# Performance work log

Measured on AMD Instinct MI355X. Metric: run time of the kernel, lower is better.

The kernel has to match this reference:

```python
import jax, jax.numpy as jnp
import numpy as np

N, D, K = 65536, 128, 2048
ENTROPY_TEMP = 0.01


def setup_inputs() -> dict:
    key = jax.random.key(0)
    k1, k2 = jax.random.split(key, 2)
    x = jax.random.normal(k1, (N, D), dtype=jnp.float32)
    mask = jnp.ones((N,), dtype=jnp.float32)
    # variance_scaling(1.0, fan_in, uniform): U(-sqrt(3/fan_in), sqrt(3/fan_in))
    lim = np.sqrt(3.0 / D).astype(np.float32)
    codebook = jax.random.uniform(k2, (K, D), dtype=jnp.float32, minval=-lim, maxval=lim)
    return {"x": x, "mask": mask, "codebook": codebook}


def _entropy_loss(affinity, mask, temperature):
    # affinity: (N, K), mask: (N,)
    aff = affinity * mask[:, None] + (1.0 - mask[:, None]) * (-100000.0)
    aff = aff / temperature
    probs = jax.nn.softmax(aff, axis=-1)
    log_probs = jax.nn.log_softmax(aff + 1e-5, axis=-1)
    target_probs = probs  # loss_type == 'softmax'
    msum = jnp.sum(mask)
    avg_probs = jnp.sum(target_probs * mask[:, None], axis=0) / msum
    avg_entropy = -jnp.sum(avg_probs * jnp.log(avg_probs + 1e-5))
    sample_entropy = -jnp.sum(jnp.sum(target_probs * log_probs, axis=-1) * mask) / msum
    return sample_entropy - avg_entropy


def reference(x, mask, codebook):
    # --- l2_norm branch: normalize x rows ---
    xn = x + (1.0 - mask)[:, None] * 1e-6
    xn = xn / jnp.maximum(jnp.linalg.norm(xn, axis=-1, keepdims=True), 1e-6)
    # squared euclidean distance with a2 = b2 = 1.0 (per the l2_norm branch)
    distances = 2.0 - 2.0 * jnp.matmul(xn, codebook.T)  # (N, K)
    logits = -distances
    encoding_indices = jnp.argmax(logits, axis=-1)  # (N,)
    # quantize: one_hot @ codebook == gather
    quantized = jnp.take(codebook, encoding_indices, axis=0)  # (N, D)
    denom = jnp.sum(mask) + 1e-6
    # per-token squared distance between unit-norm vectors: 2 - 2 * <a, b>
    e_latent_loss = jnp.sum((2.0 - 2.0 * jnp.sum(jax.lax.stop_gradient(quantized) * xn, axis=-1)) * mask) / denom
    q_latent_loss = jnp.sum((2.0 - 2.0 * jnp.sum(quantized * jax.lax.stop_gradient(xn), axis=-1)) * mask) / denom
    entropy_loss = _entropy_loss(-distances, mask, ENTROPY_TEMP)
    # straight-through estimator
    quantized_st = xn + jax.lax.stop_gradient(quantized - xn)
    # bincount with float weights == segment_sum of mask
    code_count = jax.ops.segment_sum(mask, encoding_indices, num_segments=K).astype(jnp.float32)
    return (quantized_st,
            jnp.asarray(e_latent_loss, jnp.float32),
            jnp.asarray(q_latent_loss, jnp.float32),
            jnp.asarray(entropy_loss, jnp.float32),
            code_count,
            encoding_indices)
```

## Files before the change

kernel.cpp:

```cpp
#include <hip/hip_runtime.h>
#include <math.h>

#define NTOK 65536
#define DIMD 128
#define KCB  2048
#define NSLAB 512

typedef unsigned short u16;
typedef __attribute__((ext_vector_type(8))) unsigned short u16x8;
typedef __attribute__((ext_vector_type(8))) __bf16 bf16x8;
typedef __attribute__((ext_vector_type(4))) float f32x4;

union U8 { u16x8 u; bf16x8 b; };

__device__ __forceinline__ u16 f2bf(float f) {
  union { float f; unsigned u; } c; c.f = f;
  unsigned r = c.u + 0x7FFFu + ((c.u >> 16) & 1u);
  return (u16)(r >> 16);
}
__device__ __forceinline__ float keyval(int k) {
  union { int i; float f; } c; c.i = k & 0xFFFFF800;
  return c.f;
}
__device__ __forceinline__ int imax(int a, int b) { return a > b ? a : b; }
__device__ __forceinline__ int imin(int a, int b) { return a < b ? a : b; }

__device__ __forceinline__ void stage4(const char* srcLane, char* ldsWaveBase) {
  #pragma unroll
  for (int i = 0; i < 4; ++i)
    __builtin_amdgcn_global_load_lds((const __attribute__((address_space(1))) void*)(srcLane + i * 4096),
                                     (__attribute__((address_space(3))) void*)(ldsWaveBase + i * 4096), 16, 0, 0);
}


__global__ __launch_bounds__(256) void k_packcb(const float* __restrict__ cb, u16* __restrict__ cbp,
                                                float* __restrict__ acc4) {
  const int gid = blockIdx.x * 256 + threadIdx.x;
  if (gid == 0) { acc4[0] = 0.0f; acc4[1] = 0.0f; acc4[2] = 0.0f; acc4[3] = 0.0f; }
  if (gid >= 32768) return;
  const int lane = gid & 63;
  const int f = (gid >> 6) & 15;
  const int T = gid >> 10;
  const int ks = f >> 2, nf = f & 3;
  const int hi = lane >> 4, l15 = lane & 15;
  const int c = T * 64 + nf * 16 + l15;
  const int d0 = ks * 32 + hi * 8;
  const float4 v0 = *(const float4*)(cb + (size_t)c * DIMD + d0);
  const float4 v1 = *(const float4*)(cb + (size_t)c * DIMD + d0 + 4);
  const float e[8] = {v0.x, v0.y, v0.z, v0.w, v1.x, v1.y, v1.z, v1.w};
  union { u16 s[8]; u16x8 u; } oh;
  #pragma unroll
  for (int i = 0; i < 8; ++i) oh.s[i] = f2bf(e[i]);
  u16* tile = cbp + (size_t)T * 8192;
  *(u16x8*)(tile + (f * 64 + lane) * 8) = oh.u;
}


__global__ __launch_bounds__(256, 4) void k_pass1(const float* __restrict__ x, const float* __restrict__ mask,
                                                  const float* __restrict__ cb, const u16* __restrict__ cbp,
                                                  float* __restrict__ outQ, float* __restrict__ outEnc,
                                                  float* __restrict__ apPart, float* __restrict__ cnPart,
                                                  float* __restrict__ acc4) {
  __shared__ __align__(16) char Bsmem[32768];
  const int tid = threadIdx.x;
  const int lane = tid & 63, w = tid >> 6;
  const int l15 = lane & 15, hi = lane >> 4;
  const int row0 = blockIdx.x * 128;
  const char* src = (const char*)cbp;

  U8 Ah[2][4];
  #pragma unroll
  for (int mf = 0; mf < 2; ++mf) {
    const int row = row0 + w * 32 + mf * 16 + l15;
    const float add = (1.0f - mask[row]) * 1e-6f;
    const float* xr = x + (size_t)row * DIMD + hi * 8;
    float xf[4][8];
    float ss = 0.f;
    #pragma unroll
    for (int ks = 0; ks < 4; ++ks) {
      const float4 a = *(const float4*)(xr + ks * 32);
      const float4 bq = *(const float4*)(xr + ks * 32 + 4);
      xf[ks][0] = a.x + add;  xf[ks][1] = a.y + add;  xf[ks][2] = a.z + add;  xf[ks][3] = a.w + add;
      xf[ks][4] = bq.x + add; xf[ks][5] = bq.y + add; xf[ks][6] = bq.z + add; xf[ks][7] = bq.w + add;
      #pragma unroll
      for (int e = 0; e < 8; ++e) ss = fmaf(xf[ks][e], xf[ks][e], ss);
    }
    ss += __shfl_xor(ss, 16, 64);
    ss += __shfl_xor(ss, 32, 64);
    const float sc = 1.0f / fmaxf(sqrtf(ss), 1e-6f);
    #pragma unroll
    for (int ks = 0; ks < 4; ++ks) {
      union { u16 s[8]; u16x8 u; } th;
      #pragma unroll
      for (int e = 0; e < 8; ++e) th.s[e] = f2bf(xf[ks][e] * sc);
      Ah[mf][ks].u = th.u;
    }
  }

  int kv1[8], kv2[8];
  #pragma unroll
  for (int r = 0; r < 8; ++r) { kv1[r] = 0x80000000; kv2[r] = 0x80000000; }

  stage4(src + 0 * 16384 + tid * 16, Bsmem + 0 * 16384 + w * 1024);

  for (int t = 0; t < 32; ++t) {
    const int b = t & 1;
    asm volatile("s_waitcnt vmcnt(0)" ::: "memory");
    __builtin_amdgcn_sched_barrier(0);
    __builtin_amdgcn_s_barrier();
    __builtin_amdgcn_sched_barrier(0);
    if (t < 31)
      stage4(src + (size_t)(t + 1) * 16384 + tid * 16, Bsmem + (b ^ 1) * 16384 + w * 1024);

    const char* base = Bsmem + b * 16384 + lane * 16;
    f32x4 acc[2][4];
    #pragma unroll
    for (int m = 0; m < 2; ++m)
      #pragma unroll
      for (int nf = 0; nf < 4; ++nf) acc[m][nf] = (f32x4){0.f, 0.f, 0.f, 0.f};

    __builtin_amdgcn_s_setprio(1);
    #pragma unroll
    for (int ks = 0; ks < 4; ++ks) {
      #pragma unroll
      for (int nf = 0; nf < 4; ++nf) {
        U8 bh;
        bh.u = *(const u16x8*)(base + ((ks * 4 + nf) << 10));
        acc[0][nf] = __builtin_amdgcn_mfma_f32_16x16x32_bf16(Ah[0][ks].b, bh.b, acc[0][nf], 0, 0, 0);
        acc[1][nf] = __builtin_amdgcn_mfma_f32_16x16x32_bf16(Ah[1][ks].b, bh.b, acc[1][nf], 0, 0, 0);
      }
    }
    __builtin_amdgcn_s_setprio(0);

    const int base11 = t * 64 + l15;
    #pragma unroll
    for (int m = 0; m < 2; ++m)
      #pragma unroll
      for (int rg = 0; rg < 4; ++rg) {
        const int r = m * 4 + rg;
        int kk[4];
        #pragma unroll
        for (int nf = 0; nf < 4; ++nf) {
          union { float f; int i; } cv;
          cv.f = acc[m][nf][rg];
          kk[nf] = (cv.i & 0xFFFFF800) | (base11 + nf * 16);
        }
        const int h1 = imax(kk[0], kk[1]), lo1 = imin(kk[0], kk[1]);
        const int h2 = imax(kk[2], kk[3]), lo2 = imin(kk[2], kk[3]);
        const int t1 = imax(h1, h2);
        const int t2 = imax(imin(h1, h2), (h1 > h2) ? lo1 : lo2);
        kv2[r] = imax(imax(kv2[r], t2), imin(kv1[r], t1));
        kv1[r] = imax(kv1[r], t1);
      }
  }

  __syncthreads();
  float* apLds = (float*)Bsmem;
  float* cnLds = (float*)Bsmem + KCB;
  float* smr = (float*)Bsmem + 2 * KCB;
  for (int i = tid; i < 2 * KCB; i += 256) ((float*)Bsmem)[i] = 0.0f;
  __syncthreads();

  float msum = 0.f, slat = 0.f, sent = 0.f;
  #pragma unroll
  for (int m = 0; m < 2; ++m)
    #pragma unroll
    for (int rg = 0; rg < 4; ++rg) {
      const int r = m * 4 + rg;
      int a1k = kv1[r];
      #pragma unroll
      for (int off = 1; off <= 8; off <<= 1) {
        const int ok = __shfl_xor(a1k, off, 64);
        a1k = ok > a1k ? ok : a1k;
      }
      const float a1val = keyval(a1k);
      const float val1 = keyval(kv1[r]);
      const float val2 = keyval(kv2[r]);
      const int row = row0 + w * 32 + m * 16 + hi * 4 + rg;
      const float mk = mask[row];
      const float add = (1.0f - mk) * 1e-6f;
      const float* xr = x + (size_t)row * DIMD + l15 * 8;
      const float4 xa = *(const float4*)xr;
      const float4 xb = *(const float4*)(xr + 4);
      float xs0[8] = {xa.x + add, xa.y + add, xa.z + add, xa.w + add,
                      xb.x + add, xb.y + add, xb.z + add, xb.w + add};
      float ss = 0.f;
      #pragma unroll
      for (int e = 0; e < 8; ++e) ss = fmaf(xs0[e], xs0[e], ss);
      #pragma unroll
      for (int off = 1; off <= 8; off <<= 1) ss += __shfl_xor(ss, off, 64);
      const float sc = 1.0f / fmaxf(sqrtf(ss), 1e-6f);
      const float RT = 4e-3f;
      const bool f1 = val1 > a1val - RT;
      const bool f2 = val2 > a1val - RT;
      const unsigned long long b1 = __ballot(f1);
      const unsigned long long b2 = __ballot(f2);
      unsigned m1 = (unsigned)((b1 >> (hi * 16)) & 0xFFFFull);
      unsigned m2 = (unsigned)((b2 >> (hi * 16)) & 0xFFFFull);
      float bestd = -1e30f;
      int bestk = 0x7fffffff;
      while (m1) {
        const int s = __builtin_ctz(m1); m1 &= m1 - 1;
        const int kc = __shfl(kv1[r], (hi << 4) | s, 64) & 2047;
        const float* cr = cb + (size_t)kc * DIMD + l15 * 8;
        const float4 ca = *(const float4*)cr;
        const float4 cbv = *(const float4*)(cr + 4);
        float d = xs0[0] * ca.x;
        d = fmaf(xs0[1], ca.y, d); d = fmaf(xs0[2], ca.z, d); d = fmaf(xs0[3], ca.w, d);
        d = fmaf(xs0[4], cbv.x, d); d = fmaf(xs0[5], cbv.y, d);
        d = fmaf(xs0[6], cbv.z, d); d = fmaf(xs0[7], cbv.w, d);
        #pragma unroll
        for (int off = 1; off <= 8; off <<= 1) d += __shfl_xor(d, off, 64);
        if (d > bestd || (d == bestd && kc < bestk)) { bestd = d; bestk = kc; }
      }
      while (m2) {
        const int s = __builtin_ctz(m2); m2 &= m2 - 1;
        const int kc = __shfl(kv2[r], (hi << 4) | s, 64) & 2047;
        const float* cr = cb + (size_t)kc * DIMD + l15 * 8;
        const float4 ca = *(const float4*)cr;
        const float4 cbv = *(const float4*)(cr + 4);
        float d = xs0[0] * ca.x;
        d = fmaf(xs0[1], ca.y, d); d = fmaf(xs0[2], ca.z, d); d = fmaf(xs0[3], ca.w, d);
        d = fmaf(xs0[4], cbv.x, d); d = fmaf(xs0[5], cbv.y, d);
        d = fmaf(xs0[6], cbv.z, d); d = fmaf(xs0[7], cbv.w, d);
        #pragma unroll
        for (int off = 1; off <= 8; off <<= 1) d += __shfl_xor(d, off, 64);
        if (d > bestd || (d == bestd && kc < bestk)) { bestd = d; bestk = kc; }
      }
      const float bestv = bestd * sc;
      float q = 0.f, qd = 0.f;
      if (val1 > a1val - 0.055f) {
        const float d = 200.f * (val1 - a1val);
        q = __expf(d);
        qd = q * d;
      }
      float Z = q, S = qd;
      #pragma unroll
      for (int off = 1; off <= 8; off <<= 1) {
        Z += __shfl_xor(Z, off, 64);
        S += __shfl_xor(S, off, 64);
      }
      if (q > 0.f) atomicAdd(&apLds[kv1[r] & 2047], mk * q / Z);
      const float4 g0 = *(const float4*)(cb + (size_t)bestk * DIMD + l15 * 8);
      const float4 g1 = *(const float4*)(cb + (size_t)bestk * DIMD + l15 * 8 + 4);
      *(float4*)(outQ + (size_t)row * DIMD + l15 * 8) = g0;
      *(float4*)(outQ + (size_t)row * DIMD + l15 * 8 + 4) = g1;
      if (l15 == 0) {
        atomicAdd(&cnLds[bestk], mk);
        outEnc[row] = (float)bestk;
        msum += mk;
        slat = fmaf(mk, 2.0f - 2.0f * bestv, slat);
        sent = fmaf(mk, __logf(Z) - S / Z, sent);
      }
    }
  #pragma unroll
  for (int off = 32; off; off >>= 1) {
    msum += __shfl_xor(msum, off, 64);
    slat += __shfl_xor(slat, off, 64);
    sent += __shfl_xor(sent, off, 64);
  }
  if (lane == 0) { smr[w * 3] = msum; smr[w * 3 + 1] = slat; smr[w * 3 + 2] = sent; }
  __syncthreads();
  if (tid == 0) {
    float t0 = 0.f, t1 = 0.f, t2 = 0.f;
    #pragma unroll
    for (int v = 0; v < 4; ++v) { t0 += smr[v * 3]; t1 += smr[v * 3 + 1]; t2 += smr[v * 3 + 2]; }
    atomicAdd(&acc4[0], t0);
    atomicAdd(&acc4[1], t1);
    atomicAdd(&acc4[2], t2);
  }
  float* apDst = apPart + (size_t)blockIdx.x * KCB;
  float* cnDst = cnPart + (size_t)blockIdx.x * KCB;
  for (int i = tid; i < KCB; i += 256) {
    apDst[i] = apLds[i];
    cnDst[i] = cnLds[i];
  }
}

__global__ __launch_bounds__(256) void k_reduce(const float* __restrict__ apPart, const float* __restrict__ cnPart,
                                                const float* __restrict__ acc4In, float* __restrict__ outCnt,
                                                float* __restrict__ acc4) {
  __shared__ float sa8[8][32];
  __shared__ float sc8[8][32];
  const int tid = threadIdx.x;
  const int kloc = tid & 31, sg = tid >> 5;
  const int k = blockIdx.x * 32 + kloc;
  float sa = 0.f, sc = 0.f;
  #pragma unroll
  for (int i = 0; i < 64; ++i) {
    const int s = sg * 64 + i;
    sa += apPart[(size_t)s * KCB + k];
    sc += cnPart[(size_t)s * KCB + k];
  }
  sa8[sg][kloc] = sa;
  sc8[sg][kloc] = sc;
  __syncthreads();
  if (tid < 32) {
    float ta = 0.f, tc = 0.f;
    #pragma unroll
    for (int g = 0; g < 8; ++g) { ta += sa8[g][tid]; tc += sc8[g][tid]; }
    outCnt[blockIdx.x * 32 + tid] = tc;
    const float a = ta / acc4In[0];
    float ae = a * __logf(a + 1e-5f);
    #pragma unroll
    for (int off = 1; off <= 16; off <<= 1) ae += __shfl_xor(ae, off, 64);
    if (tid == 0) atomicAdd(&acc4[3], ae);
  }
}

__global__ __launch_bounds__(64) void k_final(const float* __restrict__ acc4, float* __restrict__ out3) {
  if (threadIdx.x == 0) {
    const float msum = acc4[0];
    const float lat = acc4[1] / (msum + 1e-6f);
    out3[0] = lat;
    out3[1] = lat;
    out3[2] = acc4[2] / msum + acc4[3];
  }
}


extern "C" void kernel_launch(void* const* d_in, const int* in_sizes, int n_in,
                              void* d_out, int out_size, void* d_ws, size_t ws_size,
                              hipStream_t stream) {
  const float* x = (const float*)d_in[0];
  const float* mask = (const float*)d_in[1];
  const float* cb = (const float*)d_in[2];

  float* out = (float*)d_out;
  float* outQ = out;
  float* out3 = out + (size_t)NTOK * DIMD;
  float* outCnt = out3 + 3;
  float* outEnc = outCnt + KCB;

  float* ws = (float*)d_ws;
  float* acc4 = ws;
  u16* cbp = (u16*)(acc4 + 8);
  float* apPart = (float*)(cbp + (size_t)KCB * DIMD);
  float* cnPart = apPart + (size_t)NSLAB * KCB;

  k_packcb<<<32768 / 256, 256, 0, stream>>>(cb, cbp, acc4);
  k_pass1<<<NTOK / 128, 256, 0, stream>>>(x, mask, cb, cbp, outQ, outEnc, apPart, cnPart, acc4);
  k_reduce<<<64, 256, 0, stream>>>(apPart, cnPart, acc4, outCnt, acc4);
  k_final<<<1, 64, 0, stream>>>(acc4, out3);
}
```

Before: 104.3 us.

## Split pass-1 work across 8 waves with 16 rows each instead of 4×32

The main kernel now launches 512 threads per block, and each of the 8 waves owns 16 token rows instead of 32. Accumulator and top-2 key registers are halved, and the codebook tile staging is spread over twice as many threads, each issuing 2 loads instead of 4. The aim is more waves in flight to hide LDS, global and epilogue latency. In exchange, each codebook B fragment read from LDS now feeds one MFMA instead of two, which doubles LDS read traffic per FLOP.

```diff
diff --git a/kernel.cpp b/kernel.cpp
--- a/kernel.cpp
+++ b/kernel.cpp
@@ -25,11 +25,11 @@
 __device__ __forceinline__ int imax(int a, int b) { return a > b ? a : b; }
 __device__ __forceinline__ int imin(int a, int b) { return a < b ? a : b; }
 
-__device__ __forceinline__ void stage4(const char* srcLane, char* ldsWaveBase) {
-  #pragma unroll
-  for (int i = 0; i < 4; ++i)
-    __builtin_amdgcn_global_load_lds((const __attribute__((address_space(1))) void*)(srcLane + i * 4096),
-                                     (__attribute__((address_space(3))) void*)(ldsWaveBase + i * 4096), 16, 0, 0);
+__device__ __forceinline__ void stage2x(const char* srcLane, char* ldsWaveBase) {
+  #pragma unroll
+  for (int i = 0; i < 2; ++i)
+    __builtin_amdgcn_global_load_lds((const __attribute__((address_space(1))) void*)(srcLane + i * 8192),
+                                     (__attribute__((address_space(3))) void*)(ldsWaveBase + i * 8192), 16, 0, 0);
 }
 
 
@@ -56,7 +56,7 @@
 }
 
 
-__global__ __launch_bounds__(256, 4) void k_pass1(const float* __restrict__ x, const float* __restrict__ mask,
+__global__ __launch_bounds__(512, 2) void k_pass1(const float* __restrict__ x, const float* __restrict__ mask,
                                                   const float* __restrict__ cb, const u16* __restrict__ cbp,
                                                   float* __restrict__ outQ, float* __restrict__ outEnc,
                                                   float* __restrict__ apPart, float* __restrict__ cnPart,
@@ -68,10 +68,9 @@
   const int row0 = blockIdx.x * 128;
   const char* src = (const char*)cbp;
 
-  U8 Ah[2][4];
-  #pragma unroll
-  for (int mf = 0; mf < 2; ++mf) {
-    const int row = row0 + w * 32 + mf * 16 + l15;
+  U8 Ah[4];
+  {
+    const int row = row0 + w * 16 + l15;
     const float add = (1.0f - mask[row]) * 1e-6f;
     const float* xr = x + (size_t)row * DIMD + hi * 8;
     float xf[4][8];
@@ -93,15 +92,15 @@
       union { u16 s[8]; u16x8 u; } th;
       #pragma unroll
       for (int e = 0; e < 8; ++e) th.s[e] = f2bf(xf[ks][e] * sc);
-      Ah[mf][ks].u = th.u;
-    }
-  }
-
-  int kv1[8], kv2[8];
-  #pragma unroll
-  for (int r = 0; r < 8; ++r) { kv1[r] = 0x80000000; kv2[r] = 0x80000000; }
-
-  stage4(src + 0 * 16384 + tid * 16, Bsmem + 0 * 16384 + w * 1024);
+      Ah[ks].u = th.u;
+    }
+  }
+
+  int kv1[4], kv2[4];
+  #pragma unroll
+  for (int r = 0; r < 4; ++r) { kv1[r] = 0x80000000; kv2[r] = 0x80000000; }
+
+  stage2x(src + 0 * 16384 + tid * 16, Bsmem + 0 * 16384 + (tid >> 6) * 1024 + 0);
 
   for (int t = 0; t < 32; ++t) {
     const int b = t & 1;
@@ -110,14 +109,12 @@
     __builtin_amdgcn_s_barrier();
     __builtin_amdgcn_sched_barrier(0);
     if (t < 31)
-      stage4(src + (size_t)(t + 1) * 16384 + tid * 16, Bsmem + (b ^ 1) * 16384 + w * 1024);
+      stage2x(src + (size_t)(t + 1) * 16384 + tid * 16, Bsmem + (b ^ 1) * 16384 + w * 1024);
 
     const char* base = Bsmem + b * 16384 + lane * 16;
-    f32x4 acc[2][4];
-    #pragma unroll
-    for (int m = 0; m < 2; ++m)
-      #pragma unroll
-      for (int nf = 0; nf < 4; ++nf) acc[m][nf] = (f32x4){0.f, 0.f, 0.f, 0.f};
+    f32x4 acc[4];
+    #pragma unroll
+    for (int nf = 0; nf < 4; ++nf) acc[nf] = (f32x4){0.f, 0.f, 0.f, 0.f};
 
     __builtin_amdgcn_s_setprio(1);
     #pragma unroll
@@ -126,133 +123,126 @@
       for (int nf = 0; nf < 4; ++nf) {
         U8 bh;
         bh.u = *(const u16x8*)(base + ((ks * 4 + nf) << 10));
-        acc[0][nf] = __builtin_amdgcn_mfma_f32_16x16x32_bf16(Ah[0][ks].b, bh.b, acc[0][nf], 0, 0, 0);
-        acc[1][nf] = __builtin_amdgcn_mfma_f32_16x16x32_bf16(Ah[1][ks].b, bh.b, acc[1][nf], 0, 0, 0);
+        acc[nf] = __builtin_amdgcn_mfma_f32_16x16x32_bf16(Ah[ks].b, bh.b, acc[nf], 0, 0, 0);
       }
     }
     __builtin_amdgcn_s_setprio(0);
 
     const int base11 = t * 64 + l15;
     #pragma unroll
-    for (int m = 0; m < 2; ++m)
-      #pragma unroll
-      for (int rg = 0; rg < 4; ++rg) {
-        const int r = m * 4 + rg;
-        int kk[4];
-        #pragma unroll
-        for (int nf = 0; nf < 4; ++nf) {
-          union { float f; int i; } cv;
-          cv.f = acc[m][nf][rg];
-          kk[nf] = (cv.i & 0xFFFFF800) | (base11 + nf * 16);
-        }
-        const int h1 = imax(kk[0], kk[1]), lo1 = imin(kk[0], kk[1]);
-        const int h2 = imax(kk[2], kk[3]), lo2 = imin(kk[2], kk[3]);
-        const int t1 = imax(h1, h2);
-        const int t2 = imax(imin(h1, h2), (h1 > h2) ? lo1 : lo2);
-        kv2[r] = imax(imax(kv2[r], t2), imin(kv1[r], t1));
-        kv1[r] = imax(kv1[r], t1);
+    for (int rg = 0; rg < 4; ++rg) {
+      int kk[4];
+      #pragma unroll
+      for (int nf = 0; nf < 4; ++nf) {
+        union { float f; int i; } cv;
+        cv.f = acc[nf][rg];
+        kk[nf] = (cv.i & 0xFFFFF800) | (base11 + nf * 16);
       }
+      const int h1 = imax(kk[0], kk[1]), lo1 = imin(kk[0], kk[1]);
+      const int h2 = imax(kk[2], kk[3]), lo2 = imin(kk[2], kk[3]);
+      const int t1 = imax(h1, h2);
+      const int t2 = imax(imin(h1, h2), (h1 > h2) ? lo1 : lo2);
+      kv2[rg] = imax(imax(kv2[rg], t2), imin(kv1[rg], t1));
+      kv1[rg] = imax(kv1[rg], t1);
+    }
   }
 
   __syncthreads();
   float* apLds = (float*)Bsmem;
   float* cnLds = (float*)Bsmem + KCB;
   float* smr = (float*)Bsmem + 2 * KCB;
-  for (int i = tid; i < 2 * KCB; i += 256) ((float*)Bsmem)[i] = 0.0f;
+  for (int i = tid; i < 2 * KCB; i += 512) ((float*)Bsmem)[i] = 0.0f;
   __syncthreads();
 
   float msum = 0.f, slat = 0.f, sent = 0.f;
   #pragma unroll
-  for (int m = 0; m < 2; ++m)
-    #pragma unroll
-    for (int rg = 0; rg < 4; ++rg) {
-      const int r = m * 4 + rg;
-      int a1k = kv1[r];
-      #pragma unroll
-      for (int off = 1; off <= 8; off <<= 1) {
-        const int ok = __shfl_xor(a1k, off, 64);
-        a1k = ok > a1k ? ok : a1k;
-      }
-      const float a1val = keyval(a1k);
-      const float val1 = keyval(kv1[r]);
-      const float val2 = keyval(kv2[r]);
-      const int row = row0 + w * 32 + m * 16 + hi * 4 + rg;
-      const float mk = mask[row];
-      const float add = (1.0f - mk) * 1e-6f;
-      const float* xr = x + (size_t)row * DIMD + l15 * 8;
-      const float4 xa = *(const float4*)xr;
-      const float4 xb = *(const float4*)(xr + 4);
-      float xs0[8] = {xa.x + add, xa.y + add, xa.z + add, xa.w + add,
-                      xb.x + add, xb.y + add, xb.z + add, xb.w + add};
-      float ss = 0.f;
-      #pragma unroll
-      for (int e = 0; e < 8; ++e) ss = fmaf(xs0[e], xs0[e], ss);
-      #pragma unroll
-      for (int off = 1; off <= 8; off <<= 1) ss += __shfl_xor(ss, off, 64);
-      const float sc = 1.0f / fmaxf(sqrtf(ss), 1e-6f);
-      const float RT = 4e-3f;
-      const bool f1 = val1 > a1val - RT;
-      const bool f2 = val2 > a1val - RT;
-      const unsigned long long b1 = __ballot(f1);
-      const unsigned long long b2 = __ballot(f2);
-      unsigned m1 = (unsigned)((b1 >> (hi * 16)) & 0xFFFFull);
-      unsigned m2 = (unsigned)((b2 >> (hi * 16)) & 0xFFFFull);
-      float bestd = -1e30f;
-      int bestk = 0x7fffffff;
-      while (m1) {
-        const int s = __builtin_ctz(m1); m1 &= m1 - 1;
-        const int kc = __shfl(kv1[r], (hi << 4) | s, 64) & 2047;
-        const float* cr = cb + (size_t)kc * DIMD + l15 * 8;
-        const float4 ca = *(const float4*)cr;
-        const float4 cbv = *(const float4*)(cr + 4);
-        float d = xs0[0] * ca.x;
-        d = fmaf(xs0[1], ca.y, d); d = fmaf(xs0[2], ca.z, d); d = fmaf(xs0[3], ca.w, d);
-        d = fmaf(xs0[4], cbv.x, d); d = fmaf(xs0[5], cbv.y, d);
-        d = fmaf(xs0[6], cbv.z, d); d = fmaf(xs0[7], cbv.w, d);
-        #pragma unroll
-        for (int off = 1; off <= 8; off <<= 1) d += __shfl_xor(d, off, 64);
-        if (d > bestd || (d == bestd && kc < bestk)) { bestd = d; bestk = kc; }
-      }
-      while (m2) {
-        const int s = __builtin_ctz(m2); m2 &= m2 - 1;
-        const int kc = __shfl(kv2[r], (hi << 4) | s, 64) & 2047;
-        const float* cr = cb + (size_t)kc * DIMD + l15 * 8;
-        const float4 ca = *(const float4*)cr;
-        const float4 cbv = *(const float4*)(cr + 4);
-        float d = xs0[0] * ca.x;
-        d = fmaf(xs0[1], ca.y, d); d = fmaf(xs0[2], ca.z, d); d = fmaf(xs0[3], ca.w, d);
-        d = fmaf(xs0[4], cbv.x, d); d = fmaf(xs0[5], cbv.y, d);
-        d = fmaf(xs0[6], cbv.z, d); d = fmaf(xs0[7], cbv.w, d);
-        #pragma unroll
-        for (int off = 1; off <= 8; off <<= 1) d += __shfl_xor(d, off, 64);
-        if (d > bestd || (d == bestd && kc < bestk)) { bestd = d; bestk = kc; }
-      }
-      const float bestv = bestd * sc;
-      float q = 0.f, qd = 0.f;
-      if (val1 > a1val - 0.055f) {
-        const float d = 200.f * (val1 - a1val);
-        q = __expf(d);
-        qd = q * d;
-      }
-      float Z = q, S = qd;
-      #pragma unroll
-      for (int off = 1; off <= 8; off <<= 1) {
-        Z += __shfl_xor(Z, off, 64);
-        S += __shfl_xor(S, off, 64);
-      }
-      if (q > 0.f) atomicAdd(&apLds[kv1[r] & 2047], mk * q / Z);
-      const float4 g0 = *(const float4*)(cb + (size_t)bestk * DIMD + l15 * 8);
-      const float4 g1 = *(const float4*)(cb + (size_t)bestk * DIMD + l15 * 8 + 4);
-      *(float4*)(outQ + (size_t)row * DIMD + l15 * 8) = g0;
-      *(float4*)(outQ + (size_t)row * DIMD + l15 * 8 + 4) = g1;
-      if (l15 == 0) {
-        atomicAdd(&cnLds[bestk], mk);
-        outEnc[row] = (float)bestk;
-        msum += mk;
-        slat = fmaf(mk, 2.0f - 2.0f * bestv, slat);
-        sent = fmaf(mk, __logf(Z) - S / Z, sent);
-      }
-    }
+  for (int rg = 0; rg < 4; ++rg) {
+    int a1k = kv1[rg];
+    #pragma unroll
+    for (int off = 1; off <= 8; off <<= 1) {
+      const int ok = __shfl_xor(a1k, off, 64);
+      a1k = ok > a1k ? ok : a1k;
+    }
+    const float a1val = keyval(a1k);
+    const float val1 = keyval(kv1[rg]);
+    const float val2 = keyval(kv2[rg]);
+    const int row = row0 + w * 16 + hi * 4 + rg;
+    const float mk = mask[row];
+    const float add = (1.0f - mk) * 1e-6f;
+    const float* xr = x + (size_t)row * DIMD + l15 * 8;
+    const float4 xa = *(const float4*)xr;
+    const float4 xb = *(const float4*)(xr + 4);
+    float xs0[8] = {xa.x + add, xa.y + add, xa.z + add, xa.w + add,
+                    xb.x + add, xb.y + add, xb.z + add, xb.w + add};
+    float ss = 0.f;
+    #pragma unroll
+    for (int e = 0; e < 8; ++e) ss = fmaf(xs0[e], xs0[e], ss);
+    #pragma unroll
+    for (int off = 1; off <= 8; off <<= 1) ss += __shfl_xor(ss, off, 64);
+    const float sc = 1.0f / fmaxf(sqrtf(ss), 1e-6f);
+    const float RT = 4e-3f;
+    const bool f1 = val1 > a1val - RT;
+    const bool f2 = val2 > a1val - RT;
+    const unsigned long long b1 = __ballot(f1);
+    const unsigned long long b2 = __ballot(f2);
+    unsigned m1 = (unsigned)((b1 >> (hi * 16)) & 0xFFFFull);
+    unsigned m2 = (unsigned)((b2 >> (hi * 16)) & 0xFFFFull);
+    float bestd = -1e30f;
+    int bestk = 0x7fffffff;
+    while (m1) {
+      const int s = __builtin_ctz(m1); m1 &= m1 - 1;
+      const int kc = __shfl(kv1[rg], (hi << 4) | s, 64) & 2047;
+      const float* cr = cb + (size_t)kc * DIMD + l15 * 8;
+      const float4 ca = *(const float4*)cr;
+      const float4 cbv = *(const float4*)(cr + 4);
+      float d = xs0[0] * ca.x;
+      d = fmaf(xs0[1], ca.y, d); d = fmaf(xs0[2], ca.z, d); d = fmaf(xs0[3], ca.w, d);
+      d = fmaf(xs0[4], cbv.x, d); d = fmaf(xs0[5], cbv.y, d);
+      d = fmaf(xs0[6], cbv.z, d); d = fmaf(xs0[7], cbv.w, d);
+      #pragma unroll
+      for (int off = 1; off <= 8; off <<= 1) d += __shfl_xor(d, off, 64);
+      if (d > bestd || (d == bestd && kc < bestk)) { bestd = d; bestk = kc; }
+    }
+    while (m2) {
+      const int s = __builtin_ctz(m2); m2 &= m2 - 1;
+      const int kc = __shfl(kv2[rg], (hi << 4) | s, 64) & 2047;
+      const float* cr = cb + (size_t)kc * DIMD + l15 * 8;
+      const float4 ca = *(const float4*)cr;
+      const float4 cbv = *(const float4*)(cr + 4);
+      float d = xs0[0] * ca.x;
+      d = fmaf(xs0[1], ca.y, d); d = fmaf(xs0[2], ca.z, d); d = fmaf(xs0[3], ca.w, d);
+      d = fmaf(xs0[4], cbv.x, d); d = fmaf(xs0[5], cbv.y, d);
+      d = fmaf(xs0[6], cbv.z, d); d = fmaf(xs0[7], cbv.w, d);
+      #pragma unroll
+      for (int off = 1; off <= 8; off <<= 1) d += __shfl_xor(d, off, 64);
+      if (d > bestd || (d == bestd && kc < bestk)) { bestd = d; bestk = kc; }
+    }
+    const float bestv = bestd * sc;
+    float q = 0.f, qd = 0.f;
+    if (val1 > a1val - 0.055f) {
+      const float d = 200.f * (val1 - a1val);
+      q = __expf(d);
+      qd = q * d;
+    }
+    float Z = q, S = qd;
+    #pragma unroll
+    for (int off = 1; off <= 8; off <<= 1) {
+      Z += __shfl_xor(Z, off, 64);
+      S += __shfl_xor(S, off, 64);
+    }
+    if (q > 0.f) atomicAdd(&apLds[kv1[rg] & 2047], mk * q / Z);
+    const float4 g0 = *(const float4*)(cb + (size_t)bestk * DIMD + l15 * 8);
+    const float4 g1 = *(const float4*)(cb + (size_t)bestk * DIMD + l15 * 8 + 4);
+    *(float4*)(outQ + (size_t)row * DIMD + l15 * 8) = g0;
+    *(float4*)(outQ + (size_t)row * DIMD + l15 * 8 + 4) = g1;
+    if (l15 == 0) {
+      atomicAdd(&cnLds[bestk], mk);
+      outEnc[row] = (float)bestk;
+      msum += mk;
+      slat = fmaf(mk, 2.0f - 2.0f * bestv, slat);
+      sent = fmaf(mk, __logf(Z) - S / Z, sent);
+    }
+  }
   #pragma unroll
   for (int off = 32; off; off >>= 1) {
     msum += __shfl_xor(msum, off, 64);
@@ -264,14 +254,14 @@
   if (tid == 0) {
     float t0 = 0.f, t1 = 0.f, t2 = 0.f;
     #pragma unroll
-    for (int v = 0; v < 4; ++v) { t0 += smr[v * 3]; t1 += smr[v * 3 + 1]; t2 += smr[v * 3 + 2]; }
+    for (int v = 0; v < 8; ++v) { t0 += smr[v * 3]; t1 += smr[v * 3 + 1]; t2 += smr[v * 3 + 2]; }
     atomicAdd(&acc4[0], t0);
     atomicAdd(&acc4[1], t1);
     atomicAdd(&acc4[2], t2);
   }
   float* apDst = apPart + (size_t)blockIdx.x * KCB;
   float* cnDst = cnPart + (size_t)blockIdx.x * KCB;
-  for (int i = tid; i < KCB; i += 256) {
+  for (int i = tid; i < KCB; i += 512) {
     apDst[i] = apLds[i];
     cnDst[i] = cnLds[i];
   }
@@ -339,7 +329,7 @@
   float* cnPart = apPart + (size_t)NSLAB * KCB;
 
   k_packcb<<<32768 / 256, 256, 0, stream>>>(cb, cbp, acc4);
-  k_pass1<<<NTOK / 128, 256, 0, stream>>>(x, mask, cb, cbp, outQ, outEnc, apPart, cnPart, acc4);
+  k_pass1<<<NTOK / 128, 512, 0, stream>>>(x, mask, cb, cbp, outQ, outEnc, apPart, cnPart, acc4);
   k_reduce<<<64, 256, 0, stream>>>(apPart, cnPart, acc4, outCnt, acc4);
   k_final<<<1, 64, 0, stream>>>(acc4, out3);
 }
```

Result: faster. 97.11 us (-6.9%).

## Split codebook sweep across two blocks per tile and move tail to separate kernel

Applied to the files above, without the earlier changes.

The fused pass is split in two. A sweep kernel launches twice as many blocks, each covering half the codebook for 128 rows, and writes top-2 packed keys per lane to a global buffer. A new tail kernel reads those 64 candidates per row with one wavefront per row, then does the exact rescoring, the softmax and entropy terms, the gather and the per-slab histograms. The aim is more parallelism and better occupancy in the MFMA sweep, with a lighter tail. The cost is an extra global round-trip of 16 MB of candidate keys and one more kernel launch.

```diff
diff --git a/kernel.cpp b/kernel.cpp
--- a/kernel.cpp
+++ b/kernel.cpp
@@ -4,7 +4,7 @@
 #define NTOK 65536
 #define DIMD 128
 #define KCB  2048
-#define NSLAB 512
+#define TSLAB 256
 
 typedef unsigned short u16;
 typedef __attribute__((ext_vector_type(8))) unsigned short u16x8;
@@ -56,17 +56,15 @@
 }
 
 
-__global__ __launch_bounds__(256, 4) void k_pass1(const float* __restrict__ x, const float* __restrict__ mask,
-                                                  const float* __restrict__ cb, const u16* __restrict__ cbp,
-                                                  float* __restrict__ outQ, float* __restrict__ outEnc,
-                                                  float* __restrict__ apPart, float* __restrict__ cnPart,
-                                                  float* __restrict__ acc4) {
+__global__ __launch_bounds__(256, 4) void k_sweep(const float* __restrict__ x, const float* __restrict__ mask,
+                                                  const u16* __restrict__ cbp, int* __restrict__ kvBuf) {
   __shared__ __align__(16) char Bsmem[32768];
   const int tid = threadIdx.x;
   const int lane = tid & 63, w = tid >> 6;
   const int l15 = lane & 15, hi = lane >> 4;
-  const int row0 = blockIdx.x * 128;
-  const char* src = (const char*)cbp;
+  const int half = blockIdx.x & 1;
+  const int row0 = (blockIdx.x >> 1) * 128;
+  const char* src = (const char*)cbp + (size_t)half * 262144;
 
   U8 Ah[2][4];
   #pragma unroll
@@ -103,13 +101,13 @@
 
   stage4(src + 0 * 16384 + tid * 16, Bsmem + 0 * 16384 + w * 1024);
 
-  for (int t = 0; t < 32; ++t) {
+  for (int t = 0; t < 16; ++t) {
     const int b = t & 1;
     asm volatile("s_waitcnt vmcnt(0)" ::: "memory");
     __builtin_amdgcn_sched_barrier(0);
     __builtin_amdgcn_s_barrier();
     __builtin_amdgcn_sched_barrier(0);
-    if (t < 31)
+    if (t < 15)
       stage4(src + (size_t)(t + 1) * 16384 + tid * 16, Bsmem + (b ^ 1) * 16384 + w * 1024);
 
     const char* base = Bsmem + b * 16384 + lane * 16;
@@ -132,7 +130,7 @@
     }
     __builtin_amdgcn_s_setprio(0);
 
-    const int base11 = t * 64 + l15;
+    const int base11 = half * 1024 + t * 64 + l15;
     #pragma unroll
     for (int m = 0; m < 2; ++m)
       #pragma unroll
@@ -154,107 +152,91 @@
       }
   }
 
-  __syncthreads();
-  float* apLds = (float*)Bsmem;
-  float* cnLds = (float*)Bsmem + KCB;
-  float* smr = (float*)Bsmem + 2 * KCB;
-  for (int i = tid; i < 2 * KCB; i += 256) ((float*)Bsmem)[i] = 0.0f;
-  __syncthreads();
-
-  float msum = 0.f, slat = 0.f, sent = 0.f;
   #pragma unroll
   for (int m = 0; m < 2; ++m)
     #pragma unroll
     for (int rg = 0; rg < 4; ++rg) {
       const int r = m * 4 + rg;
-      int a1k = kv1[r];
-      #pragma unroll
-      for (int off = 1; off <= 8; off <<= 1) {
-        const int ok = __shfl_xor(a1k, off, 64);
-        a1k = ok > a1k ? ok : a1k;
-      }
-      const float a1val = keyval(a1k);
-      const float val1 = keyval(kv1[r]);
-      const float val2 = keyval(kv2[r]);
       const int row = row0 + w * 32 + m * 16 + hi * 4 + rg;
-      const float mk = mask[row];
-      const float add = (1.0f - mk) * 1e-6f;
-      const float* xr = x + (size_t)row * DIMD + l15 * 8;
-      const float4 xa = *(const float4*)xr;
-      const float4 xb = *(const float4*)(xr + 4);
-      float xs0[8] = {xa.x + add, xa.y + add, xa.z + add, xa.w + add,
-                      xb.x + add, xb.y + add, xb.z + add, xb.w + add};
-      float ss = 0.f;
-      #pragma unroll
-      for (int e = 0; e < 8; ++e) ss = fmaf(xs0[e], xs0[e], ss);
-      #pragma unroll
-      for (int off = 1; off <= 8; off <<= 1) ss += __shfl_xor(ss, off, 64);
-      const float sc = 1.0f / fmaxf(sqrtf(ss), 1e-6f);
-      const float RT = 4e-3f;
-      const bool f1 = val1 > a1val - RT;
-      const bool f2 = val2 > a1val - RT;
-      const unsigned long long b1 = __ballot(f1);
-      const unsigned long long b2 = __ballot(f2);
-      unsigned m1 = (unsigned)((b1 >> (hi * 16)) & 0xFFFFull);
-      unsigned m2 = (unsigned)((b2 >> (hi * 16)) & 0xFFFFull);
-      float bestd = -1e30f;
-      int bestk = 0x7fffffff;
-      while (m1) {
-        const int s = __builtin_ctz(m1); m1 &= m1 - 1;
-        const int kc = __shfl(kv1[r], (hi << 4) | s, 64) & 2047;
-        const float* cr = cb + (size_t)kc * DIMD + l15 * 8;
-        const float4 ca = *(const float4*)cr;
-        const float4 cbv = *(const float4*)(cr + 4);
-        float d = xs0[0] * ca.x;
-        d = fmaf(xs0[1], ca.y, d); d = fmaf(xs0[2], ca.z, d); d = fmaf(xs0[3], ca.w, d);
-        d = fmaf(xs0[4], cbv.x, d); d = fmaf(xs0[5], cbv.y, d);
-        d = fmaf(xs0[6], cbv.z, d); d = fmaf(xs0[7], cbv.w, d);
-        #pragma unroll
-        for (int off = 1; off <= 8; off <<= 1) d += __shfl_xor(d, off, 64);
-        if (d > bestd || (d == bestd && kc < bestk)) { bestd = d; bestk = kc; }
-      }
-      while (m2) {
-        const int s = __builtin_ctz(m2); m2 &= m2 - 1;
-        const int kc = __shfl(kv2[r], (hi << 4) | s, 64) & 2047;
-        const float* cr = cb + (size_t)kc * DIMD + l15 * 8;
-        const float4 ca = *(const float4*)cr;
-        const float4 cbv = *(const float4*)(cr + 4);
-        float d = xs0[0] * ca.x;
-        d = fmaf(xs0[1], ca.y, d); d = fmaf(xs0[2], ca.z, d); d = fmaf(xs0[3], ca.w, d);
-        d = fmaf(xs0[4], cbv.x, d); d = fmaf(xs0[5], cbv.y, d);
-        d = fmaf(xs0[6], cbv.z, d); d = fmaf(xs0[7], cbv.w, d);
-        #pragma unroll
-        for (int off = 1; off <= 8; off <<= 1) d += __shfl_xor(d, off, 64);
-        if (d > bestd || (d == bestd && kc < bestk)) { bestd = d; bestk = kc; }
-      }
-      const float bestv = bestd * sc;
-      float q = 0.f, qd = 0.f;
-      if (val1 > a1val - 0.055f) {
-        const float d = 200.f * (val1 - a1val);
-        q = __expf(d);
-        qd = q * d;
-      }
-      float Z = q, S = qd;
-      #pragma unroll
-      for (int off = 1; off <= 8; off <<= 1) {
-        Z += __shfl_xor(Z, off, 64);
-        S += __shfl_xor(S, off, 64);
-      }
-      if (q > 0.f) atomicAdd(&apLds[kv1[r] & 2047], mk * q / Z);
-      const float4 g0 = *(const float4*)(cb + (size_t)bestk * DIMD + l15 * 8);
-      const float4 g1 = *(const float4*)(cb + (size_t)bestk * DIMD + l15 * 8 + 4);
-      *(float4*)(outQ + (size_t)row * DIMD + l15 * 8) = g0;
-      *(float4*)(outQ + (size_t)row * DIMD + l15 * 8 + 4) = g1;
-      if (l15 == 0) {
-        atomicAdd(&cnLds[bestk], mk);
-        outEnc[row] = (float)bestk;
-        msum += mk;
-        slat = fmaf(mk, 2.0f - 2.0f * bestv, slat);
-        sent = fmaf(mk, __logf(Z) - S / Z, sent);
-      }
-    }
-  #pragma unroll
-  for (int off = 32; off; off >>= 1) {
+      int2 kv;
+      kv.x = kv1[r];
+      kv.y = kv2[r];
+      *(int2*)(kvBuf + (size_t)row * 64 + half * 32 + l15 * 2) = kv;
+    }
+}
+
+
+__global__ __launch_bounds__(256) void k_tail(const float* __restrict__ x, const float* __restrict__ mask,
+                                              const float* __restrict__ cb, const int* __restrict__ kvBuf,
+                                              float* __restrict__ outQ, float* __restrict__ outEnc,
+                                              float* __restrict__ apPart, float* __restrict__ cnPart,
+                                              float* __restrict__ acc4) {
+  __shared__ float ap[KCB];
+  __shared__ float cn[KCB];
+  __shared__ float smr[12];
+  const int tid = threadIdx.x;
+  const int lane = tid & 63, w = tid >> 6;
+  for (int i = tid; i < KCB; i += 256) { ap[i] = 0.0f; cn[i] = 0.0f; }
+  __syncthreads();
+
+  float msum = 0.f, slat = 0.f, sent = 0.f;
+  for (int row = blockIdx.x * 4 + w; row < NTOK; row += TSLAB * 4) {
+    const int key = kvBuf[(size_t)row * 64 + lane];
+    int mx = key;
+    #pragma unroll
+    for (int off = 1; off <= 32; off <<= 1) {
+      const int ok = __shfl_xor(mx, off, 64);
+      mx = ok > mx ? ok : mx;
+    }
+    const float a1val = keyval(mx);
+    const float myval = keyval(key);
+    const float mkk = mask[row];
+    const float add = (1.0f - mkk) * 1e-6f;
+    const float2 xv = *(const float2*)(x + (size_t)row * DIMD + lane * 2);
+    const float x0 = xv.x + add, x1 = xv.y + add;
+    float ss = fmaf(x0, x0, x1 * x1);
+    #pragma unroll
+    for (int off = 1; off <= 32; off <<= 1) ss += __shfl_xor(ss, off, 64);
+    const float sc = 1.0f / fmaxf(sqrtf(ss), 1e-6f);
+    unsigned long long cmask = __ballot(myval > a1val - 4e-3f);
+    float bestd = -1e30f;
+    int bestk = 0x7fffffff;
+    while (cmask) {
+      const int s = __builtin_ctzll(cmask);
+      cmask &= cmask - 1;
+      const int kc = __shfl(key, s, 64) & 2047;
+      const float2 cv = *(const float2*)(cb + (size_t)kc * DIMD + lane * 2);
+      float d = fmaf(x0, cv.x, x1 * cv.y);
+      #pragma unroll
+      for (int off = 1; off <= 32; off <<= 1) d += __shfl_xor(d, off, 64);
+      if (d > bestd || (d == bestd && kc < bestk)) { bestd = d; bestk = kc; }
+    }
+    const float bestv = bestd * sc;
+    float q = 0.f, qd = 0.f;
+    if (myval > a1val - 0.055f) {
+      const float d = 200.f * (myval - a1val);
+      q = __expf(d);
+      qd = q * d;
+    }
+    float Z = q, S = qd;
+    #pragma unroll
+    for (int off = 1; off <= 32; off <<= 1) {
+      Z += __shfl_xor(Z, off, 64);
+      S += __shfl_xor(S, off, 64);
+    }
+    if (q > 0.f) atomicAdd(&ap[key & 2047], mkk * q / Z);
+    const float2 g = *(const float2*)(cb + (size_t)bestk * DIMD + lane * 2);
+    *(float2*)(outQ + (size_t)row * DIMD + lane * 2) = g;
+    if (lane == 0) {
+      atomicAdd(&cn[bestk], mkk);
+      outEnc[row] = (float)bestk;
+      msum += mkk;
+      slat = fmaf(mkk, 2.0f - 2.0f * bestv, slat);
+      sent = fmaf(mkk, __logf(Z) - S / Z, sent);
+    }
+  }
+  #pragma unroll
+  for (int off = 1; off <= 32; off <<= 1) {
     msum += __shfl_xor(msum, off, 64);
     slat += __shfl_xor(slat, off, 64);
     sent += __shfl_xor(sent, off, 64);
@@ -272,8 +254,8 @@
   float* apDst = apPart + (size_t)blockIdx.x * KCB;
   float* cnDst = cnPart + (size_t)blockIdx.x * KCB;
   for (int i = tid; i < KCB; i += 256) {
-    apDst[i] = apLds[i];
-    cnDst[i] = cnLds[i];
+    apDst[i] = ap[i];
+    cnDst[i] = cn[i];
   }
 }
 
@@ -287,8 +269,8 @@
   const int k = blockIdx.x * 32 + kloc;
   float sa = 0.f, sc = 0.f;
   #pragma unroll
-  for (int i = 0; i < 64; ++i) {
-    const int s = sg * 64 + i;
+  for (int i = 0; i < 32; ++i) {
+    const int s = sg * 32 + i;
     sa += apPart[(size_t)s * KCB + k];
     sc += cnPart[(size_t)s * KCB + k];
   }
@@ -335,11 +317,13 @@
   float* ws = (float*)d_ws;
   float* acc4 = ws;
   u16* cbp = (u16*)(acc4 + 8);
-  float* apPart = (float*)(cbp + (size_t)KCB * DIMD);
-  float* cnPart = apPart + (size_t)NSLAB * KCB;
+  int* kvBuf = (int*)(cbp + (size_t)KCB * DIMD);
+  float* apPart = (float*)(kvBuf + (size_t)NTOK * 64);
+  float* cnPart = apPart + (size_t)TSLAB * KCB;
 
   k_packcb<<<32768 / 256, 256, 0, stream>>>(cb, cbp, acc4);
-  k_pass1<<<NTOK / 128, 256, 0, stream>>>(x, mask, cb, cbp, outQ, outEnc, apPart, cnPart, acc4);
+  k_sweep<<<(NTOK / 128) * 2, 256, 0, stream>>>(x, mask, cbp, kvBuf);
+  k_tail<<<TSLAB, 256, 0, stream>>>(x, mask, cb, kvBuf, outQ, outEnc, apPart, cnPart, acc4);
   k_reduce<<<64, 256, 0, stream>>>(apPart, cnPart, acc4, outCnt, acc4);
   k_final<<<1, 64, 0, stream>>>(acc4, out3);
 }
```

After: 181.3 us. 73.8% more time.
